# Kernel tuning notes

Hardware: AMD Instinct MI355X
Metric: run time of the kernel (lower is better)

## Reference

```python
import jax, jax.numpy as jnp
import numpy as np

DIM = 512; H = 8; DH = 64; M = 256; ITERS = 6; K = 33  # residual conv kernel


def _pinv(x, iters=ITERS):
    # Moore-Penrose iterative pseudo-inverse (lucidrains moore_penrose_iter_pinv)
    abs_x = jnp.abs(x)
    denom = abs_x.sum(-1).max() * abs_x.sum(-2).max()  # global max of col/row sums
    z = jnp.swapaxes(x, -1, -2) / denom
    I = jnp.eye(x.shape[-1], dtype=x.dtype)
    for _ in range(iters):
        xz = x @ z
        z = 0.25 * z @ (13. * I - xz @ (15. * I - xz @ (7. * I - xz)))
    return z


def setup_inputs() -> dict:
    key = jax.random.key(0)
    ks = jax.random.split(key, 5)
    b, n = 4, 4096
    inner = H * DH
    x = jax.random.normal(ks[0], (b, n, DIM), jnp.float32)
    ln_g = jnp.ones((DIM,), jnp.float32)
    ln_b = jnp.zeros((DIM,), jnp.float32)
    w_qkv = jax.random.normal(ks[1], (DIM, 3 * inner), jnp.float32) / np.sqrt(DIM).astype(np.float32)
    w_out = jax.random.normal(ks[2], (inner, DIM), jnp.float32) / np.sqrt(inner).astype(np.float32)
    b_out = jnp.zeros((DIM,), jnp.float32)
    res_w = jax.random.normal(ks[3], (H, K), jnp.float32) * 0.02  # depthwise conv weight per head
    return {"x": x, "ln_g": ln_g, "ln_b": ln_b, "w_qkv": w_qkv,
            "w_out": w_out, "b_out": b_out, "res_w": res_w}


def reference(x, ln_g, ln_b, w_qkv, w_out, b_out, res_w):
    b, n, d = x.shape
    # LayerNorm (eps=1e-5, biased variance, like torch)
    mu = x.mean(-1, keepdims=True)
    var = ((x - mu) ** 2).mean(-1, keepdims=True)
    xn = (x - mu) * jax.lax.rsqrt(var + 1e-5) * ln_g + ln_b
    # QKV projection, no bias
    qkv = xn @ w_qkv  # [b, n, 3*h*dh]
    q, k, v = jnp.split(qkv, 3, axis=-1)
    tohd = lambda t: t.reshape(b, n, H, DH).transpose(0, 2, 1, 3)  # b h n d
    q = tohd(q) * (DH ** -0.5)
    k = tohd(k)
    v = tohd(v)
    # landmarks: mean over consecutive blocks of l = n // M (n divisible by M here)
    l = n // M
    q_l = q.reshape(b, H, M, l, DH).mean(3)  # b h m d
    k_l = k.reshape(b, H, M, l, DH).mean(3)
    attn1 = jax.nn.softmax(jnp.einsum('bhid,bhjd->bhij', q, k_l), axis=-1)   # b h n m
    attn2 = jax.nn.softmax(jnp.einsum('bhid,bhjd->bhij', q_l, k_l), axis=-1)  # b h m m
    attn3 = jax.nn.softmax(jnp.einsum('bhid,bhjd->bhij', q_l, k), axis=-1)   # b h m n
    out = (attn1 @ _pinv(attn2)) @ (attn3 @ v)  # b h n dh
    # depthwise residual conv over sequence dim (Conv2d(heads, heads, (33,1), groups=heads))
    res = jax.lax.conv_general_dilated(
        v, res_w.reshape(H, 1, K, 1), (1, 1), ((K // 2, K // 2), (0, 0)),
        feature_group_count=H, dimension_numbers=('NCHW', 'OIHW', 'NCHW'))
    out = out + res
    # merge heads + output projection (dropout is identity at eval)
    out = out.transpose(0, 2, 1, 3).reshape(b, n, H * DH) @ w_out + b_out
    # TransLayer residual
    return x + out
```

## Files before the change

### kernel.cpp

```cpp
#include <hip/hip_runtime.h>
#include <hip/hip_bf16.h>

#define SEQ    4096
#define NBAT   4
#define NHEAD  8
#define NBH    32
#define DMODEL 512
#define DHEAD  64
#define NLM    256

typedef __attribute__((ext_vector_type(8))) short s8v;
typedef __attribute__((ext_vector_type(4))) float f4v;

__device__ __forceinline__ float b2f(unsigned short u){
  union { unsigned int i; float f; } v; v.i = ((unsigned int)u) << 16; return v.f;
}
__device__ __forceinline__ unsigned short f2b(float f){
  union { float f; unsigned int i; } v; v.f = f;
  unsigned int r = v.i + 0x7fffu + ((v.i >> 16) & 1u);
  return (unsigned short)(r >> 16);
}
__device__ __forceinline__ s8v ldg8(const unsigned short* p){
  return *reinterpret_cast<const s8v*>(p);
}
__device__ __forceinline__ f4v mfma16(s8v a, s8v b, f4v c){
  return __builtin_amdgcn_mfma_f32_16x16x32_bf16(a, b, c, 0, 0, 0);
}
__device__ __forceinline__ f4v zero4(){ f4v z; z[0]=0.f; z[1]=0.f; z[2]=0.f; z[3]=0.f; return z; }
__device__ __forceinline__ void gload16(const unsigned short* g, unsigned short* l){
  __builtin_amdgcn_global_load_lds((const __attribute__((address_space(1))) unsigned int*)g,
                                   (__attribute__((address_space(3))) unsigned int*)l, 16, 0, 0);
}

__global__ void k_prep(const float* __restrict__ wqkv, const float* __restrict__ wout,
                       unsigned short* __restrict__ wqkvT, unsigned short* __restrict__ woutT,
                       unsigned int* __restrict__ denomU){
  int t = blockIdx.x*256 + threadIdx.x;
  if (t == 0) denomU[0] = 0u;
  if (t < 786432){ int kk = t/1536, n = t%1536; wqkvT[(size_t)n*512 + kk] = f2b(wqkv[t]); }
  else { int t2 = t - 786432; if (t2 < 262144){ int kk = t2/512, n = t2%512; woutT[(size_t)n*512 + kk] = f2b(wout[t2]); } }
}

__global__ __launch_bounds__(256) void k_ln(const float* __restrict__ x, const float* __restrict__ g,
                                            const float* __restrict__ be, unsigned short* __restrict__ xn){
  int row = blockIdx.x*4 + (threadIdx.x>>6);
  int l = threadIdx.x & 63;
  const float* xr = x + (size_t)row*DMODEL;
  float4 a = *(const float4*)(xr + l*4);
  float4 b = *(const float4*)(xr + 256 + l*4);
  float s = a.x+a.y+a.z+a.w + b.x+b.y+b.z+b.w;
  float q = a.x*a.x+a.y*a.y+a.z*a.z+a.w*a.w + b.x*b.x+b.y*b.y+b.z*b.z+b.w*b.w;
  #pragma unroll
  for (int m=1;m<64;m<<=1){ s += __shfl_xor(s,m); q += __shfl_xor(q,m); }
  float mean = s*(1.f/DMODEL);
  float rstd = rsqrtf(q*(1.f/DMODEL) - mean*mean + 1e-5f);
  int c0 = l*4, c1 = 256 + l*4;
  float av[4] = {a.x,a.y,a.z,a.w}, bv[4] = {b.x,b.y,b.z,b.w};
  ushort4 u0, u1;
  unsigned short* p0 = (unsigned short*)&u0; unsigned short* p1 = (unsigned short*)&u1;
  #pragma unroll
  for (int e=0;e<4;++e){
    p0[e] = f2b((av[e]-mean)*rstd*g[c0+e] + be[c0+e]);
    p1[e] = f2b((bv[e]-mean)*rstd*g[c1+e] + be[c1+e]);
  }
  *(ushort4*)(xn + (size_t)row*DMODEL + c0) = u0;
  *(ushort4*)(xn + (size_t)row*DMODEL + c1) = u1;
}

__device__ __forceinline__ void gemm512v2(const unsigned short* __restrict__ A, const unsigned short* __restrict__ B,
                                          int m0, int n0, int t, unsigned short* lA, unsigned short* lB,
                                          f4v acc[4][4]){
  int w = t>>6, l = t&63;
  int wm = (w&1)*64, wn = (w>>1)*64;
  int g = l>>4, qi = l&15;
  int rs = (w<<4) + (l>>2);
  int s0 = l&3;
  int c0 = ((s0 ^ ((rs>>1)&3)) << 3);
  int r1 = rs + 64;
  int c1 = ((s0 ^ ((r1>>1)&3)) << 3);
  const unsigned short* gA0 = A + (size_t)(m0+rs)*DMODEL + c0;
  const unsigned short* gA1 = A + (size_t)(m0+r1)*DMODEL + c1;
  const unsigned short* gB0 = B + (size_t)(n0+rs)*DMODEL + c0;
  const unsigned short* gB1 = B + (size_t)(n0+r1)*DMODEL + c1;
  unsigned short* dA0 = lA + (w<<9);
  unsigned short* dA1 = lA + 2048 + (w<<9);
  unsigned short* dB0 = lB + (w<<9);
  unsigned short* dB1 = lB + 2048 + (w<<9);
  int aofs[4], bofs[4];
  #pragma unroll
  for (int i=0;i<4;++i){
    int ra = wm + i*16 + qi;
    aofs[i] = ra*32 + ((g ^ ((ra>>1)&3))<<3);
    int rb = wn + i*16 + qi;
    bofs[i] = rb*32 + ((g ^ ((rb>>1)&3))<<3);
  }
  for (int ks=0; ks<16; ++ks){
    gload16(gA0, dA0); gload16(gA1, dA1);
    gload16(gB0, dB0); gload16(gB1, dB1);
    gA0 += 32; gA1 += 32; gB0 += 32; gB1 += 32;
    __syncthreads();
    s8v af[4], bf[4];
    #pragma unroll
    for (int i=0;i<4;++i) af[i] = *(s8v*)&lA[aofs[i]];
    #pragma unroll
    for (int j=0;j<4;++j) bf[j] = *(s8v*)&lB[bofs[j]];
    #pragma unroll
    for (int i=0;i<4;++i)
      #pragma unroll
      for (int j=0;j<4;++j) acc[i][j] = mfma16(af[i], bf[j], acc[i][j]);
    __syncthreads();
  }
}

__global__ __launch_bounds__(256) void k_gqkv(const unsigned short* __restrict__ xn, const unsigned short* __restrict__ wT,
                                              unsigned short* __restrict__ q, unsigned short* __restrict__ k,
                                              unsigned short* __restrict__ v, unsigned short* __restrict__ vT){
  __shared__ __align__(16) unsigned short lA[4096], lB[4096];
  int bid = blockIdx.x; int mblk = bid/12, nblk = bid%12;
  int m0 = mblk*128, n0 = nblk*128;
  int t = threadIdx.x;
  f4v acc[4][4];
  #pragma unroll
  for (int i=0;i<4;++i)
    #pragma unroll
    for (int j=0;j<4;++j) acc[i][j] = zero4();
  gemm512v2(xn, wT, m0, n0, t, lA, lB, acc);
  int w = t>>6, l = t&63; int wm = (w&1)*64, wn = (w>>1)*64;
  int part = nblk >> 2;
  int coff = (nblk & 3) * 128;
  unsigned short* dst = (part==0) ? q : (part==1) ? k : v;
  float scale = (part==0) ? 0.125f : 1.f;
  #pragma unroll
  for (int i=0;i<4;++i)
  #pragma unroll
  for (int j=0;j<4;++j){
    int colg = coff + wn + j*16 + (l&15);
    int h = colg>>6, c = colg&63;
    #pragma unroll
    for (int r=0;r<4;++r){
      int rowg = m0 + wm + i*16 + ((l>>4)<<2) + r;
      int b = rowg>>12, n = rowg&4095;
      unsigned short val = f2b(acc[i][j][r]*scale);
      dst[ (((size_t)(b*NHEAD + h))*SEQ + n)*DHEAD + c ] = val;
      if (part == 2)
        vT[ (((size_t)(b*NHEAD + h))*DHEAD + c)*SEQ + n ] = val;
    }
  }
}

__global__ __launch_bounds__(256) void k_gout(const unsigned short* __restrict__ ao, const unsigned short* __restrict__ wT,
                                              const float* __restrict__ x, const float* __restrict__ bo,
                                              float* __restrict__ out){
  __shared__ __align__(16) unsigned short lA[4096], lB[4096];
  int bid = blockIdx.x; int mblk = bid>>2, nblk = bid&3;
  int m0 = mblk*128, n0 = nblk*128;
  int t = threadIdx.x;
  f4v acc[4][4];
  #pragma unroll
  for (int i=0;i<4;++i)
    #pragma unroll
    for (int j=0;j<4;++j) acc[i][j] = zero4();
  gemm512v2(ao, wT, m0, n0, t, lA, lB, acc);
  int w = t>>6, l = t&63; int wm = (w&1)*64, wn = (w>>1)*64;
  #pragma unroll
  for (int i=0;i<4;++i)
  #pragma unroll
  for (int j=0;j<4;++j){
    int colg = n0 + wn + j*16 + (l&15);
    #pragma unroll
    for (int r=0;r<4;++r){
      int rowg = m0 + wm + i*16 + ((l>>4)<<2) + r;
      size_t ad = (size_t)rowg*DMODEL + colg;
      out[ad] = acc[i][j][r] + x[ad] + bo[colg];
    }
  }
}

__global__ void k_lmk(const unsigned short* __restrict__ q, const unsigned short* __restrict__ k,
                      unsigned short* __restrict__ ql, unsigned short* __restrict__ kl){
  int tg = blockIdx.x*256 + threadIdx.x;
  int c4 = (tg&15)*4, m = (tg>>4)&255, bh = tg>>12;
  const unsigned short* qb = q + ((size_t)bh*SEQ + m*16)*DHEAD + c4;
  const unsigned short* kb = k + ((size_t)bh*SEQ + m*16)*DHEAD + c4;
  float s0=0.f,s1=0.f,s2=0.f,s3=0.f, t0=0.f,t1=0.f,t2=0.f,t3=0.f;
  #pragma unroll
  for (int j=0;j<16;++j){
    ushort4 uq = *(const ushort4*)(qb + (size_t)j*DHEAD);
    ushort4 uk = *(const ushort4*)(kb + (size_t)j*DHEAD);
    s0+=b2f(uq.x); s1+=b2f(uq.y); s2+=b2f(uq.z); s3+=b2f(uq.w);
    t0+=b2f(uk.x); t1+=b2f(uk.y); t2+=b2f(uk.z); t3+=b2f(uk.w);
  }
  ushort4 oq, ok;
  oq.x=f2b(s0*(1.f/16.f)); oq.y=f2b(s1*(1.f/16.f)); oq.z=f2b(s2*(1.f/16.f)); oq.w=f2b(s3*(1.f/16.f));
  ok.x=f2b(t0*(1.f/16.f)); ok.y=f2b(t1*(1.f/16.f)); ok.z=f2b(t2*(1.f/16.f)); ok.w=f2b(t3*(1.f/16.f));
  *(ushort4*)(ql + ((size_t)bh*NLM + m)*DHEAD + c4) = oq;
  *(ushort4*)(kl + ((size_t)bh*NLM + m)*DHEAD + c4) = ok;
}

__global__ __launch_bounds__(512) void k_attn2(const unsigned short* __restrict__ ql, const unsigned short* __restrict__ kl,
                                               unsigned short* __restrict__ a2, unsigned short* __restrict__ a2t,
                                               unsigned int* __restrict__ denomU){
  __shared__ float cs[256];
  int bh = blockIdx.x; int t = threadIdx.x; int w = t>>6, l = t&63;
  const unsigned short* Q = ql + (size_t)bh*NLM*DHEAD;
  const unsigned short* K = kl + (size_t)bh*NLM*DHEAD;
  f4v acc[2][16];
  #pragma unroll
  for (int i=0;i<2;++i)
    #pragma unroll
    for (int j=0;j<16;++j) acc[i][j] = zero4();
  int m0 = w*32;
  #pragma unroll
  for (int ks=0; ks<2; ++ks){
    int kk = ks*32 + ((l>>4)<<3);
    s8v af0 = ldg8(&Q[(size_t)(m0 + (l&15))*DHEAD + kk]);
    s8v af1 = ldg8(&Q[(size_t)(m0 + 16 + (l&15))*DHEAD + kk]);
    #pragma unroll
    for (int j=0;j<16;++j){
      s8v bf = ldg8(&K[(size_t)(j*16 + (l&15))*DHEAD + kk]);
      acc[0][j] = mfma16(af0, bf, acc[0][j]);
      acc[1][j] = mfma16(af1, bf, acc[1][j]);
    }
  }
  #pragma unroll
  for (int i=0;i<2;++i)
  #pragma unroll
  for (int r=0;r<4;++r){
    float mx = -1e30f;
    #pragma unroll
    for (int j=0;j<16;++j) mx = fmaxf(mx, acc[i][j][r]);
    #pragma unroll
    for (int mm=1;mm<16;mm<<=1) mx = fmaxf(mx, __shfl_xor(mx,mm));
    float sm = 0.f;
    #pragma unroll
    for (int j=0;j<16;++j){ float p = __expf(acc[i][j][r]-mx); acc[i][j][r]=p; sm += p; }
    #pragma unroll
    for (int mm=1;mm<16;mm<<=1) sm += __shfl_xor(sm,mm);
    float inv = 1.f/sm;
    #pragma unroll
    for (int j=0;j<16;++j) acc[i][j][r] *= inv;
  }
  for (int e=t; e<256; e+=512) cs[e] = 0.f;
  __syncthreads();
  size_t b0 = (size_t)bh*NLM*NLM;
  #pragma unroll
  for (int i=0;i<2;++i)
  #pragma unroll
  for (int j=0;j<16;++j){
    int col = j*16 + (l&15);
    int rowb = m0 + i*16 + ((l>>4)<<2);
    float csp = 0.f;
    #pragma unroll
    for (int r=0;r<4;++r){
      float p = acc[i][j][r];
      unsigned short pb = f2b(p);
      a2 [b0 + (size_t)(rowb+r)*NLM + col] = pb;
      a2t[b0 + (size_t)col*NLM + rowb + r] = pb;
      csp += p;
    }
    csp += __shfl_xor(csp, 16); csp += __shfl_xor(csp, 32);
    if ((l>>4) == 0) atomicAdd(&cs[col], csp);
  }
  __syncthreads();
  if (t < 256) atomicMax(denomU, __float_as_uint(cs[t]));
}

__global__ __launch_bounds__(128) void k_a3w2(const unsigned short* __restrict__ ql, const unsigned short* __restrict__ kb,
                                              const unsigned short* __restrict__ vT, unsigned short* __restrict__ w2t){
  int bh = blockIdx.x >> 3;
  int t = threadIdx.x, w = t>>6, l = t&63;
  int q0 = ((blockIdx.x & 7) << 5) + (w<<4);
  int g = l>>4, qi = l&15;
  const unsigned short* Q = ql + ((size_t)bh*NLM + q0)*DHEAD;
  const unsigned short* K = kb + (size_t)bh*SEQ*DHEAD;
  const unsigned short* V = vT + (size_t)bh*DHEAD*SEQ;
  float m_run = -1e30f, den = 0.f;
  f4v oacc[4];
  #pragma unroll
  for (int j=0;j<4;++j) oacc[j] = zero4();
  int sl0 = ((g&1)*2)*16 + qi;
  int jsel = g>>1;
  for (int kc=0; kc<16; ++kc){
    const unsigned short* Kc = K + (size_t)kc*256*DHEAD;
    f4v acc[16];
    #pragma unroll
    for (int j=0;j<16;++j) acc[j] = zero4();
    #pragma unroll
    for (int ks=0;ks<2;++ks){
      int kk = ks*32 + g*8;
      s8v bq = ldg8(&Q[(size_t)qi*DHEAD + kk]);
      #pragma unroll
      for (int j=0;j<16;++j){
        s8v ak = ldg8(&Kc[(size_t)(j*16+qi)*DHEAD + kk]);
        acc[j] = mfma16(ak, bq, acc[j]);
      }
    }
    float cm = -1e30f;
    #pragma unroll
    for (int j=0;j<16;++j)
      cm = fmaxf(cm, fmaxf(fmaxf(acc[j][0],acc[j][1]), fmaxf(acc[j][2],acc[j][3])));
    cm = fmaxf(cm, __shfl_xor(cm,16));
    cm = fmaxf(cm, __shfl_xor(cm,32));
    float nm = fmaxf(m_run, cm);
    float f = __expf(m_run - nm);
    m_run = nm;
    float ls = 0.f;
    unsigned int pku[32];
    #pragma unroll
    for (int j=0;j<16;++j){
      float p0 = __expf(acc[j][0]-nm), p1 = __expf(acc[j][1]-nm);
      float p2 = __expf(acc[j][2]-nm), p3 = __expf(acc[j][3]-nm);
      ls += (p0+p1)+(p2+p3);
      pku[2*j+0] = (unsigned int)f2b(p0) | ((unsigned int)f2b(p1)<<16);
      pku[2*j+1] = (unsigned int)f2b(p2) | ((unsigned int)f2b(p3)<<16);
    }
    den = den*f + ls;
    float fr0 = __shfl(f, g*4+0, 64), fr1 = __shfl(f, g*4+1, 64);
    float fr2 = __shfl(f, g*4+2, 64), fr3 = __shfl(f, g*4+3, 64);
    #pragma unroll
    for (int j=0;j<4;++j){
      oacc[j][0]*=fr0; oacc[j][1]*=fr1; oacc[j][2]*=fr2; oacc[j][3]*=fr3;
    }
    #pragma unroll
    for (int ks=0;ks<8;++ks){
      unsigned int w0a = (unsigned int)__shfl((int)pku[4*ks+0], sl0, 64);
      unsigned int w1a = (unsigned int)__shfl((int)pku[4*ks+1], sl0, 64);
      unsigned int w0b = (unsigned int)__shfl((int)pku[4*ks+2], sl0, 64);
      unsigned int w1b = (unsigned int)__shfl((int)pku[4*ks+3], sl0, 64);
      unsigned int w2a = (unsigned int)__shfl((int)pku[4*ks+0], sl0+16, 64);
      unsigned int w3a = (unsigned int)__shfl((int)pku[4*ks+1], sl0+16, 64);
      unsigned int w2b = (unsigned int)__shfl((int)pku[4*ks+2], sl0+16, 64);
      unsigned int w3b = (unsigned int)__shfl((int)pku[4*ks+3], sl0+16, 64);
      unsigned int wv0 = jsel ? w0b : w0a;
      unsigned int wv1 = jsel ? w1b : w1a;
      unsigned int wv2 = jsel ? w2b : w2a;
      unsigned int wv3 = jsel ? w3b : w3a;
      s8v af;
      af[0] = (short)(wv0&0xffff); af[1] = (short)(wv0>>16);
      af[2] = (short)(wv1&0xffff); af[3] = (short)(wv1>>16);
      af[4] = (short)(wv2&0xffff); af[5] = (short)(wv2>>16);
      af[6] = (short)(wv3&0xffff); af[7] = (short)(wv3>>16);
      int mk = ks*32 + g*8;
      #pragma unroll
      for (int j=0;j<4;++j){
        s8v bu = ldg8(&V[(size_t)(j*16+qi)*SEQ + kc*256 + mk]);
        oacc[j] = mfma16(af, bu, oacc[j]);
      }
    }
  }
  den += __shfl_xor(den,16); den += __shfl_xor(den,32);
  float inv = 1.f/den;
  float ir0 = __shfl(inv, g*4+0, 64), ir1 = __shfl(inv, g*4+1, 64);
  float ir2 = __shfl(inv, g*4+2, 64), ir3 = __shfl(inv, g*4+3, 64);
  #pragma unroll
  for (int j=0;j<4;++j){
    size_t cb = ((size_t)bh*DHEAD + j*16 + qi)*NLM + q0 + g*4;
    w2t[cb+0] = f2b(oacc[j][0]*ir0);
    w2t[cb+1] = f2b(oacc[j][1]*ir1);
    w2t[cb+2] = f2b(oacc[j][2]*ir2);
    w2t[cb+3] = f2b(oacc[j][3]*ir3);
  }
}

__global__ __launch_bounds__(256) void k_conv(const unsigned short* __restrict__ v, const float* __restrict__ rw,
                                              unsigned short* __restrict__ cf){
  int bh = blockIdx.x >> 6;
  int n0 = (blockIdx.x & 63) * 64;
  int h = bh & 7, b = bh >> 3;
  int t = threadIdx.x;
  int tx = t & 15, ty = t >> 4;
  int c4 = tx * 4;
  int nb = n0 + ty * 4;
  const unsigned short* vb = v + ((size_t)bh * SEQ) * DHEAD + c4;
  ushort4 val[36];
  #pragma unroll
  for (int i = 0; i < 36; ++i){
    int nn = nb - 16 + i;
    if (nn >= 0 && nn < SEQ) val[i] = *(const ushort4*)(vb + (size_t)nn * DHEAD);
    else { val[i].x = 0; val[i].y = 0; val[i].z = 0; val[i].w = 0; }
  }
  float wgt[33];
  #pragma unroll
  for (int o = 0; o < 33; ++o) wgt[o] = rw[h*33 + o];
  #pragma unroll
  for (int i = 0; i < 4; ++i){
    float s0 = 0.f, s1 = 0.f, s2 = 0.f, s3 = 0.f;
    #pragma unroll
    for (int o = 0; o < 33; ++o){
      ushort4 u = val[i + o];
      float w0 = wgt[o];
      s0 += w0 * b2f(u.x); s1 += w0 * b2f(u.y);
      s2 += w0 * b2f(u.z); s3 += w0 * b2f(u.w);
    }
    ushort4 ov;
    ov.x = f2b(s0); ov.y = f2b(s1); ov.z = f2b(s2); ov.w = f2b(s3);
    size_t ad = ((size_t)b * SEQ + (nb + i)) * DMODEL + h * DHEAD + c4;
    *(ushort4*)(cf + ad) = ov;
  }
}

__device__ __forceinline__ void pcore(const unsigned short* __restrict__ Ab, const unsigned short* __restrict__ Bb,
                                      int m0, int n0, int l, f4v acc[4][4]){
  for (int ks=0; ks<8; ++ks){
    int kk = ks*32 + ((l>>4)<<3);
    s8v af[4], bf[4];
    #pragma unroll
    for (int i=0;i<4;++i) af[i] = ldg8(&Ab[(size_t)(m0 + i*16 + (l&15))*256 + kk]);
    #pragma unroll
    for (int j=0;j<4;++j) bf[j] = ldg8(&Bb[(size_t)(n0 + j*16 + (l&15))*256 + kk]);
    #pragma unroll
    for (int i=0;i<4;++i)
      #pragma unroll
      for (int j=0;j<4;++j) acc[i][j] = mfma16(af[i], bf[j], acc[i][j]);
  }
}

__global__ __launch_bounds__(64) void k_pg1(const unsigned short* __restrict__ A, const unsigned short* __restrict__ BT,
                                            unsigned short* __restrict__ oN, unsigned short* __restrict__ oT,
                                            int sdiv, const unsigned int* __restrict__ denomU){
  int bid = blockIdx.x;
  int bh = bid>>4, tt = bid&15;
  int m0 = (tt>>2)*64, n0 = (tt&3)*64;
  int l = threadIdx.x;
  const unsigned short* Ab = A + (size_t)bh*65536;
  const unsigned short* Bb = BT + (size_t)bh*65536;
  f4v acc[4][4];
  #pragma unroll
  for (int i=0;i<4;++i)
    #pragma unroll
    for (int j=0;j<4;++j) acc[i][j] = zero4();
  pcore(Ab, Bb, m0, n0, l, acc);
  float s = sdiv ? 1.f/__uint_as_float(denomU[0]) : 1.f;
  #pragma unroll
  for (int i=0;i<4;++i)
  #pragma unroll
  for (int j=0;j<4;++j){
    int col = n0 + j*16 + (l&15);
    #pragma unroll
    for (int r=0;r<4;++r){
      int row = m0 + i*16 + ((l>>4)<<2) + r;
      unsigned short ob = f2b(acc[i][j][r]*s);
      oN[(size_t)bh*65536 + (size_t)row*256 + col] = ob;
      oT[(size_t)bh*65536 + (size_t)col*256 + row] = ob;
    }
  }
}

__global__ __launch_bounds__(64) void k_pg2(const unsigned short* __restrict__ xzN, const unsigned short* __restrict__ xzT,
                                            const unsigned short* __restrict__ zsrc,
                                            unsigned short* __restrict__ CT, unsigned short* __restrict__ PN,
                                            int sdiv, const unsigned int* __restrict__ denomU){
  int bid = blockIdx.x;
  int part = bid>>9; bid &= 511;
  int bh = bid>>4, tt = bid&15;
  int m0 = (tt>>2)*64, n0 = (tt&3)*64;
  int l = threadIdx.x;
  const unsigned short* Ab = (part==0 ? xzN : zsrc) + (size_t)bh*65536;
  const unsigned short* Bb = xzT + (size_t)bh*65536;
  f4v acc[4][4];
  #pragma unroll
  for (int i=0;i<4;++i)
    #pragma unroll
    for (int j=0;j<4;++j) acc[i][j] = zero4();
  pcore(Ab, Bb, m0, n0, l, acc);
  if (part == 0){
    #pragma unroll
    for (int i=0;i<4;++i)
    #pragma unroll
    for (int j=0;j<4;++j){
      int col = n0 + j*16 + (l&15);
      #pragma unroll
      for (int r=0;r<4;++r){
        int row = m0 + i*16 + ((l>>4)<<2) + r;
        float xv = b2f(xzN[(size_t)bh*65536 + (size_t)row*256 + col]);
        CT[(size_t)bh*65536 + (size_t)col*256 + row] = f2b(7.f*xv - acc[i][j][r]);
      }
    }
  } else {
    float s = sdiv ? 1.f/__uint_as_float(denomU[0]) : 1.f;
    #pragma unroll
    for (int i=0;i<4;++i)
    #pragma unroll
    for (int j=0;j<4;++j){
      int col = n0 + j*16 + (l&15);
      #pragma unroll
      for (int r=0;r<4;++r){
        int row = m0 + i*16 + ((l>>4)<<2) + r;
        PN[(size_t)bh*65536 + (size_t)row*256 + col] = f2b(acc[i][j][r]*s);
      }
    }
  }
}

__global__ __launch_bounds__(64) void k_pg3(const unsigned short* __restrict__ PN, const unsigned short* __restrict__ CT,
                                            const unsigned short* __restrict__ zsrc,
                                            unsigned short* __restrict__ zN, unsigned short* __restrict__ zT,
                                            int sdiv, const unsigned int* __restrict__ denomU){
  int bid = blockIdx.x;
  int bh = bid>>4, tt = bid&15;
  int m0 = (tt>>2)*64, n0 = (tt&3)*64;
  int l = threadIdx.x;
  const unsigned short* Ab = PN + (size_t)bh*65536;
  const unsigned short* Bb = CT + (size_t)bh*65536;
  f4v acc[4][4];
  #pragma unroll
  for (int i=0;i<4;++i)
    #pragma unroll
    for (int j=0;j<4;++j) acc[i][j] = zero4();
  pcore(Ab, Bb, m0, n0, l, acc);
  float zs = sdiv ? 1.f/__uint_as_float(denomU[0]) : 1.f;
  #pragma unroll
  for (int i=0;i<4;++i)
  #pragma unroll
  for (int j=0;j<4;++j){
    int col = n0 + j*16 + (l&15);
    #pragma unroll
    for (int r=0;r<4;++r){
      int row = m0 + i*16 + ((l>>4)<<2) + r;
      float zv = b2f(zsrc[(size_t)bh*65536 + (size_t)row*256 + col])*zs;
      float pv = b2f(PN  [(size_t)bh*65536 + (size_t)row*256 + col]);
      float res = 0.25f*(13.f*zv - 15.f*pv + acc[i][j][r]);
      unsigned short ob = f2b(res);
      zN[(size_t)bh*65536 + (size_t)row*256 + col] = ob;
      zT[(size_t)bh*65536 + (size_t)col*256 + row] = ob;
    }
  }
}

template<bool WN, bool WT>
__global__ __launch_bounds__(64) void k_pgemm(
    const unsigned short* __restrict__ A, const unsigned short* __restrict__ BT,
    unsigned short* __restrict__ oN, unsigned short* __restrict__ oT,
    int mt, int nt, long strA, long strBT, long strON, long strOT)
{
  int bid = blockIdx.x;
  int nper = mt*nt;
  int bh = bid/nper, tt = bid%nper;
  int m0 = (tt/nt)*64, n0 = (tt%nt)*64;
  const unsigned short* Ab = A + (size_t)bh*strA;
  const unsigned short* Bb = BT + (size_t)bh*strBT;
  int l = threadIdx.x;
  f4v acc[4][4];
  #pragma unroll
  for (int i=0;i<4;++i)
    #pragma unroll
    for (int j=0;j<4;++j) acc[i][j] = zero4();
  pcore(Ab, Bb, m0, n0, l, acc);
  #pragma unroll
  for (int i=0;i<4;++i)
  #pragma unroll
  for (int j=0;j<4;++j){
    int col = n0 + j*16 + (l&15);
    #pragma unroll
    for (int r=0;r<4;++r){
      int row = m0 + i*16 + ((l>>4)<<2) + r;
      unsigned short ob = f2b(acc[i][j][r]);
      if constexpr (WN) oN[(size_t)bh*strON + (size_t)row*256 + col] = ob;
      if constexpr (WT) oT[(size_t)bh*strOT + (size_t)col*256 + row] = ob;
    }
  }
}

__global__ __launch_bounds__(256) void k_attn1(const unsigned short* __restrict__ qb, const unsigned short* __restrict__ kl,
                                               const unsigned short* __restrict__ ut, const unsigned short* __restrict__ cf,
                                               unsigned short* __restrict__ ao){
  int bh = blockIdx.x>>6;
  int t = threadIdx.x, w = t>>6, l = t&63;
  int q0 = ((blockIdx.x&63)<<6) + (w<<4);
  int g = l>>4, qi = l&15;
  const unsigned short* Q = qb + (size_t)bh*SEQ*DHEAD;
  const unsigned short* K = kl + (size_t)bh*NLM*DHEAD;
  f4v acc[16];
  #pragma unroll
  for (int j=0;j<16;++j) acc[j] = zero4();
  #pragma unroll
  for (int ks=0;ks<2;++ks){
    int kk = ks*32 + g*8;
    s8v bq = ldg8(&Q[(size_t)(q0+qi)*DHEAD + kk]);
    #pragma unroll
    for (int j=0;j<16;++j){
      s8v ak = ldg8(&K[(size_t)(j*16+qi)*DHEAD + kk]);
      acc[j] = mfma16(ak, bq, acc[j]);
    }
  }
  float mx = -1e30f;
  #pragma unroll
  for (int j=0;j<16;++j)
    mx = fmaxf(mx, fmaxf(fmaxf(acc[j][0],acc[j][1]), fmaxf(acc[j][2],acc[j][3])));
  mx = fmaxf(mx, __shfl_xor(mx,16));
  mx = fmaxf(mx, __shfl_xor(mx,32));
  float sm = 0.f;
  #pragma unroll
  for (int j=0;j<16;++j)
    #pragma unroll
    for (int r=0;r<4;++r){ float p = __expf(acc[j][r]-mx); acc[j][r]=p; sm += p; }
  sm += __shfl_xor(sm,16); sm += __shfl_xor(sm,32);
  float inv = 1.f/sm;
  unsigned int pku[32];
  #pragma unroll
  for (int j=0;j<16;++j){
    pku[2*j+0] = (unsigned int)f2b(acc[j][0]*inv) | ((unsigned int)f2b(acc[j][1]*inv)<<16);
    pku[2*j+1] = (unsigned int)f2b(acc[j][2]*inv) | ((unsigned int)f2b(acc[j][3]*inv)<<16);
  }
  const unsigned short* U = ut + (size_t)bh*DHEAD*NLM;
  f4v oacc[4];
  #pragma unroll
  for (int j=0;j<4;++j) oacc[j] = zero4();
  int sl0 = ((g&1)*2)*16 + qi;
  int jsel = g>>1;
  #pragma unroll
  for (int ks=0;ks<8;++ks){
    unsigned int w0a = (unsigned int)__shfl((int)pku[4*ks+0], sl0, 64);
    unsigned int w1a = (unsigned int)__shfl((int)pku[4*ks+1], sl0, 64);
    unsigned int w0b = (unsigned int)__shfl((int)pku[4*ks+2], sl0, 64);
    unsigned int w1b = (unsigned int)__shfl((int)pku[4*ks+3], sl0, 64);
    unsigned int w2a = (unsigned int)__shfl((int)pku[4*ks+0], sl0+16, 64);
    unsigned int w3a = (unsigned int)__shfl((int)pku[4*ks+1], sl0+16, 64);
    unsigned int w2b = (unsigned int)__shfl((int)pku[4*ks+2], sl0+16, 64);
    unsigned int w3b = (unsigned int)__shfl((int)pku[4*ks+3], sl0+16, 64);
    unsigned int wv0 = jsel ? w0b : w0a;
    unsigned int wv1 = jsel ? w1b : w1a;
    unsigned int wv2 = jsel ? w2b : w2a;
    unsigned int wv3 = jsel ? w3b : w3a;
    s8v af;
    af[0] = (short)(wv0&0xffff); af[1] = (short)(wv0>>16);
    af[2] = (short)(wv1&0xffff); af[3] = (short)(wv1>>16);
    af[4] = (short)(wv2&0xffff); af[5] = (short)(wv2>>16);
    af[6] = (short)(wv3&0xffff); af[7] = (short)(wv3>>16);
    int mk = ks*32 + g*8;
    #pragma unroll
    for (int j=0;j<4;++j){
      s8v bu = ldg8(&U[(size_t)(j*16+qi)*NLM + mk]);
      oacc[j] = mfma16(af, bu, oacc[j]);
    }
  }
  int b = bh>>3, h = bh&7;
  #pragma unroll
  for (int j=0;j<4;++j){
    int c = j*16 + qi;
    #pragma unroll
    for (int r=0;r<4;++r){
      int n = q0 + g*4 + r;
      size_t ad = ((size_t)(b*SEQ + n))*DMODEL + h*DHEAD + c;
      ao[ad] = f2b(oacc[j][r] + b2f(cf[ad]));
    }
  }
}

extern "C" void kernel_launch(void* const* d_in, const int* in_sizes, int n_in,
                              void* d_out, int out_size, void* d_ws, size_t ws_size,
                              hipStream_t stream){
  const float* x    = (const float*)d_in[0];
  const float* lng  = (const float*)d_in[1];
  const float* lnb  = (const float*)d_in[2];
  const float* wqkv = (const float*)d_in[3];
  const float* wout = (const float*)d_in[4];
  const float* bout = (const float*)d_in[5];
  const float* resw = (const float*)d_in[6];
  float* out = (float*)d_out;

  char* ws = (char*)d_ws;
  size_t off = 0;
  auto alloc = [&](size_t bytes)->char*{ char* p = ws + off; off += (bytes + 255) & ~(size_t)255; return p; };

  unsigned short* wqkvT = (unsigned short*)alloc((size_t)1536*512*2);
  unsigned short* woutT = (unsigned short*)alloc((size_t)512*512*2);
  unsigned int*   denomU= (unsigned int*)  alloc(256);
  unsigned short* xn    = (unsigned short*)alloc((size_t)16384*512*2);
  unsigned short* zA  = xn;
  unsigned short* zAT = xn + (size_t)1*NBH*NLM*NLM;
  unsigned short* zB  = xn + (size_t)2*NBH*NLM*NLM;
  unsigned short* zBT = xn + (size_t)3*NBH*NLM*NLM;
  unsigned short* q   = (unsigned short*)alloc((size_t)NBH*SEQ*DHEAD*2);
  unsigned short* kb  = (unsigned short*)alloc((size_t)NBH*SEQ*DHEAD*2);
  unsigned short* ao  = kb;
  unsigned short* v   = (unsigned short*)alloc((size_t)NBH*SEQ*DHEAD*2);
  unsigned short* vT  = (unsigned short*)alloc((size_t)NBH*DHEAD*SEQ*2);
  unsigned short* ql  = (unsigned short*)alloc((size_t)NBH*NLM*DHEAD*2);
  unsigned short* kl  = (unsigned short*)alloc((size_t)NBH*NLM*DHEAD*2);
  unsigned short* a2  = (unsigned short*)alloc((size_t)NBH*NLM*NLM*2);
  unsigned short* a2t = (unsigned short*)alloc((size_t)NBH*NLM*NLM*2);
  unsigned short* convf = (unsigned short*)alloc((size_t)NBAT*SEQ*DMODEL*2);
  unsigned short* xz  = (unsigned short*)alloc((size_t)NBH*NLM*NLM*2);
  unsigned short* xzt = (unsigned short*)alloc((size_t)NBH*NLM*NLM*2);
  unsigned short* pn  = (unsigned short*)alloc((size_t)NBH*NLM*NLM*2);
  unsigned short* ctb = (unsigned short*)alloc((size_t)NBH*NLM*NLM*2);
  unsigned short* w2t = (unsigned short*)alloc((size_t)NBH*DHEAD*NLM*2);
  unsigned short* ut  = (unsigned short*)alloc((size_t)NBH*DHEAD*NLM*2);
  (void)ws_size; (void)in_sizes; (void)n_in; (void)out_size;

  k_prep<<<4096,256,0,stream>>>(wqkv, wout, wqkvT, woutT, denomU);
  k_ln  <<<4096,256,0,stream>>>(x, lng, lnb, xn);
  k_gqkv<<<1536,256,0,stream>>>(xn, wqkvT, q, kb, v, vT);
  k_lmk <<<512,256,0,stream>>>(q, kb, ql, kl);
  k_attn2<<<32,512,0,stream>>>(ql, kl, a2, a2t, denomU);
  k_a3w2<<<256,128,0,stream>>>(ql, kb, vT, w2t);
  k_conv<<<2048,256,0,stream>>>(v, resw, convf);

  unsigned short* zN_[2] = {zA, zB};
  unsigned short* zT_[2] = {zAT, zBT};
  for (int it = 0; it < 6; ++it){
    const unsigned short* BT   = (it==0) ? a2  : zT_[(it-1)&1];
    const unsigned short* zsrc = (it==0) ? a2t : zN_[(it-1)&1];
    int sdiv = (it==0) ? 1 : 0;
    k_pg1<<<512 ,64,0,stream>>>(a2, BT, xz, xzt, sdiv, denomU);
    k_pg2<<<1024,64,0,stream>>>(xz, xzt, zsrc, ctb, pn, sdiv, denomU);
    k_pg3<<<512 ,64,0,stream>>>(pn, ctb, zsrc, zN_[it&1], zT_[it&1], sdiv, denomU);
  }
  k_pgemm<false,true><<<128,64,0,stream>>>(zN_[1], w2t, (unsigned short*)nullptr, ut, 4,1, 65536L,16384L,0L,16384L);

  k_attn1<<<2048,256,0,stream>>>(q, kl, ut, convf, ao);
  k_gout <<<512,256,0,stream>>>(ao, woutT, x, bout, out);
}
```

Baseline: 559.6 us.

## Split-K the attn3·V landmark kernel and widen pinv GEMM blocks to four waves

The attn3@V kernel becomes split-K with a flash-decoding style design: 1024 blocks each handle a quarter of the sequence and write float partial outputs, running maxima and denominators. A new combine kernel rescales the partials, merges them and writes w2t in bf16. The pseudo-inverse GEMM kernels and the final z·W2 GEMM now run four 16-row waves per 64x64 tile instead of one wave computing the whole tile, which adds parallelism to latency-bound small GEMMs. The cost is an extra launch, partial-buffer round trips, and each wave loading the B operand separately without LDS sharing.

```diff
diff --git a/kernel.cpp b/kernel.cpp
--- a/kernel.cpp
+++ b/kernel.cpp
@@ -265,11 +265,14 @@
   if (t < 256) atomicMax(denomU, __float_as_uint(cs[t]));
 }
 
-__global__ __launch_bounds__(128) void k_a3w2(const unsigned short* __restrict__ ql, const unsigned short* __restrict__ kb,
-                                              const unsigned short* __restrict__ vT, unsigned short* __restrict__ w2t){
-  int bh = blockIdx.x >> 3;
+__global__ __launch_bounds__(128) void k_a3w2p(const unsigned short* __restrict__ ql, const unsigned short* __restrict__ kb,
+                                               const unsigned short* __restrict__ vT,
+                                               float* __restrict__ po, float* __restrict__ pm, float* __restrict__ pd){
+  int ksp = blockIdx.x & 3;
+  int qb  = (blockIdx.x >> 2) & 7;
+  int bh  = blockIdx.x >> 5;
   int t = threadIdx.x, w = t>>6, l = t&63;
-  int q0 = ((blockIdx.x & 7) << 5) + (w<<4);
+  int q0 = (qb<<5) + (w<<4);
   int g = l>>4, qi = l&15;
   const unsigned short* Q = ql + ((size_t)bh*NLM + q0)*DHEAD;
   const unsigned short* K = kb + (size_t)bh*SEQ*DHEAD;
@@ -280,7 +283,7 @@
   for (int j=0;j<4;++j) oacc[j] = zero4();
   int sl0 = ((g&1)*2)*16 + qi;
   int jsel = g>>1;
-  for (int kc=0; kc<16; ++kc){
+  for (int kc = ksp*4; kc < ksp*4+4; ++kc){
     const unsigned short* Kc = K + (size_t)kc*256*DHEAD;
     f4v acc[16];
     #pragma unroll
@@ -349,17 +352,40 @@
     }
   }
   den += __shfl_xor(den,16); den += __shfl_xor(den,32);
-  float inv = 1.f/den;
-  float ir0 = __shfl(inv, g*4+0, 64), ir1 = __shfl(inv, g*4+1, 64);
-  float ir2 = __shfl(inv, g*4+2, 64), ir3 = __shfl(inv, g*4+3, 64);
-  #pragma unroll
-  for (int j=0;j<4;++j){
-    size_t cb = ((size_t)bh*DHEAD + j*16 + qi)*NLM + q0 + g*4;
-    w2t[cb+0] = f2b(oacc[j][0]*ir0);
-    w2t[cb+1] = f2b(oacc[j][1]*ir1);
-    w2t[cb+2] = f2b(oacc[j][2]*ir2);
-    w2t[cb+3] = f2b(oacc[j][3]*ir3);
-  }
+  #pragma unroll
+  for (int j=0;j<4;++j)
+    #pragma unroll
+    for (int r=0;r<4;++r)
+      po[(((size_t)(ksp*NBH + bh))*NLM + q0 + g*4 + r)*DHEAD + j*16 + qi] = oacc[j][r];
+  if (g == 0){
+    pm[(size_t)(ksp*NBH + bh)*NLM + q0 + qi] = m_run;
+    pd[(size_t)(ksp*NBH + bh)*NLM + q0 + qi] = den;
+  }
+}
+
+__global__ __launch_bounds__(256) void k_a3c(const float* __restrict__ po, const float* __restrict__ pm,
+                                             const float* __restrict__ pd, unsigned short* __restrict__ w2t){
+  int tg = blockIdx.x*256 + threadIdx.x;
+  int bh = tg >> 12; int c = (tg >> 6) & 63; int r4 = (tg & 63) << 2;
+  ushort4 ov;
+  unsigned short* op = (unsigned short*)&ov;
+  #pragma unroll
+  for (int rr=0; rr<4; ++rr){
+    int row = r4 + rr;
+    float m[4];
+    float gm = -1e30f;
+    #pragma unroll
+    for (int s=0;s<4;++s){ m[s] = pm[(size_t)(s*NBH+bh)*NLM + row]; gm = fmaxf(gm, m[s]); }
+    float den = 0.f, o = 0.f;
+    #pragma unroll
+    for (int s=0;s<4;++s){
+      float wsc = __expf(m[s]-gm);
+      den += pd[(size_t)(s*NBH+bh)*NLM + row]*wsc;
+      o   += po[(((size_t)(s*NBH+bh))*NLM + row)*DHEAD + c]*wsc;
+    }
+    op[rr] = f2b(o/den);
+  }
+  *(ushort4*)&w2t[(size_t)bh*DHEAD*NLM + (size_t)c*NLM + r4] = ov;
 }
 
 __global__ __launch_bounds__(256) void k_conv(const unsigned short* __restrict__ v, const float* __restrict__ rw,
@@ -399,166 +425,127 @@
   }
 }
 
-__device__ __forceinline__ void pcore(const unsigned short* __restrict__ Ab, const unsigned short* __restrict__ Bb,
-                                      int m0, int n0, int l, f4v acc[4][4]){
-  for (int ks=0; ks<8; ++ks){
-    int kk = ks*32 + ((l>>4)<<3);
-    s8v af[4], bf[4];
-    #pragma unroll
-    for (int i=0;i<4;++i) af[i] = ldg8(&Ab[(size_t)(m0 + i*16 + (l&15))*256 + kk]);
-    #pragma unroll
-    for (int j=0;j<4;++j) bf[j] = ldg8(&Bb[(size_t)(n0 + j*16 + (l&15))*256 + kk]);
-    #pragma unroll
-    for (int i=0;i<4;++i)
-      #pragma unroll
-      for (int j=0;j<4;++j) acc[i][j] = mfma16(af[i], bf[j], acc[i][j]);
-  }
-}
-
-__global__ __launch_bounds__(64) void k_pg1(const unsigned short* __restrict__ A, const unsigned short* __restrict__ BT,
-                                            unsigned short* __restrict__ oN, unsigned short* __restrict__ oT,
+__device__ __forceinline__ void grow16(const unsigned short* __restrict__ A, const unsigned short* __restrict__ BT,
+                                       int rowb, int n0, int qi, int g, f4v acc[4]){
+  #pragma unroll
+  for (int ks=0;ks<8;++ks){
+    int kk = ks*32 + g*8;
+    s8v af = ldg8(&A[(size_t)(rowb+qi)*256 + kk]);
+    #pragma unroll
+    for (int j=0;j<4;++j){
+      s8v bf = ldg8(&BT[(size_t)(n0+j*16+qi)*256 + kk]);
+      acc[j] = mfma16(af, bf, acc[j]);
+    }
+  }
+}
+
+
+__global__ __launch_bounds__(256) void k_q1(const unsigned short* __restrict__ a2, const unsigned short* __restrict__ zT,
+                                            unsigned short* __restrict__ xzN, unsigned short* __restrict__ xzT,
                                             int sdiv, const unsigned int* __restrict__ denomU){
-  int bid = blockIdx.x;
-  int bh = bid>>4, tt = bid&15;
+  int blk = blockIdx.x;
+  int t = threadIdx.x, w = t>>6, l = t&63, g = l>>4, qi = l&15;
+  int bh = blk>>4, tt = blk&15;
   int m0 = (tt>>2)*64, n0 = (tt&3)*64;
-  int l = threadIdx.x;
-  const unsigned short* Ab = A + (size_t)bh*65536;
-  const unsigned short* Bb = BT + (size_t)bh*65536;
-  f4v acc[4][4];
-  #pragma unroll
-  for (int i=0;i<4;++i)
-    #pragma unroll
-    for (int j=0;j<4;++j) acc[i][j] = zero4();
-  pcore(Ab, Bb, m0, n0, l, acc);
+  size_t bb = (size_t)bh*65536;
+  int rowb = m0 + w*16;
   float s = sdiv ? 1.f/__uint_as_float(denomU[0]) : 1.f;
-  #pragma unroll
-  for (int i=0;i<4;++i)
-  #pragma unroll
-  for (int j=0;j<4;++j){
-    int col = n0 + j*16 + (l&15);
+  f4v acc[4];
+  #pragma unroll
+  for (int j=0;j<4;++j) acc[j] = zero4();
+  grow16(a2+bb, zT+bb, rowb, n0, qi, g, acc);
+  #pragma unroll
+  for (int j=0;j<4;++j)
     #pragma unroll
     for (int r=0;r<4;++r){
-      int row = m0 + i*16 + ((l>>4)<<2) + r;
-      unsigned short ob = f2b(acc[i][j][r]*s);
-      oN[(size_t)bh*65536 + (size_t)row*256 + col] = ob;
-      oT[(size_t)bh*65536 + (size_t)col*256 + row] = ob;
-    }
-  }
-}
-
-__global__ __launch_bounds__(64) void k_pg2(const unsigned short* __restrict__ xzN, const unsigned short* __restrict__ xzT,
+      int row = rowb+g*4+r, col = n0+j*16+qi;
+      unsigned short ob = f2b(acc[j][r]*s);
+      xzN[bb + (size_t)row*256 + col] = ob;
+      xzT[bb + (size_t)col*256 + row] = ob;
+    }
+}
+
+__global__ __launch_bounds__(256) void k_q2(const unsigned short* __restrict__ xzN, const unsigned short* __restrict__ xzT,
                                             const unsigned short* __restrict__ zsrc,
                                             unsigned short* __restrict__ CT, unsigned short* __restrict__ PN,
                                             int sdiv, const unsigned int* __restrict__ denomU){
-  int bid = blockIdx.x;
-  int part = bid>>9; bid &= 511;
-  int bh = bid>>4, tt = bid&15;
+  int blk = blockIdx.x;
+  int part = blk>>9; blk &= 511;
+  int t = threadIdx.x, w = t>>6, l = t&63, g = l>>4, qi = l&15;
+  int bh = blk>>4, tt = blk&15;
   int m0 = (tt>>2)*64, n0 = (tt&3)*64;
-  int l = threadIdx.x;
-  const unsigned short* Ab = (part==0 ? xzN : zsrc) + (size_t)bh*65536;
-  const unsigned short* Bb = xzT + (size_t)bh*65536;
-  f4v acc[4][4];
-  #pragma unroll
-  for (int i=0;i<4;++i)
-    #pragma unroll
-    for (int j=0;j<4;++j) acc[i][j] = zero4();
-  pcore(Ab, Bb, m0, n0, l, acc);
+  size_t bb = (size_t)bh*65536;
+  int rowb = m0 + w*16;
+  f4v acc[4];
+  #pragma unroll
+  for (int j=0;j<4;++j) acc[j] = zero4();
   if (part == 0){
-    #pragma unroll
-    for (int i=0;i<4;++i)
-    #pragma unroll
-    for (int j=0;j<4;++j){
-      int col = n0 + j*16 + (l&15);
+    grow16(xzN+bb, xzT+bb, rowb, n0, qi, g, acc);
+    #pragma unroll
+    for (int j=0;j<4;++j)
       #pragma unroll
       for (int r=0;r<4;++r){
-        int row = m0 + i*16 + ((l>>4)<<2) + r;
-        float xv = b2f(xzN[(size_t)bh*65536 + (size_t)row*256 + col]);
-        CT[(size_t)bh*65536 + (size_t)col*256 + row] = f2b(7.f*xv - acc[i][j][r]);
+        int row = rowb+g*4+r, col = n0+j*16+qi;
+        float xv = b2f(xzN[bb + (size_t)row*256 + col]);
+        CT[bb + (size_t)col*256 + row] = f2b(7.f*xv - acc[j][r]);
       }
-    }
   } else {
+    grow16(zsrc+bb, xzT+bb, rowb, n0, qi, g, acc);
     float s = sdiv ? 1.f/__uint_as_float(denomU[0]) : 1.f;
     #pragma unroll
-    for (int i=0;i<4;++i)
-    #pragma unroll
-    for (int j=0;j<4;++j){
-      int col = n0 + j*16 + (l&15);
+    for (int j=0;j<4;++j)
       #pragma unroll
       for (int r=0;r<4;++r){
-        int row = m0 + i*16 + ((l>>4)<<2) + r;
-        PN[(size_t)bh*65536 + (size_t)row*256 + col] = f2b(acc[i][j][r]*s);
+        int row = rowb+g*4+r, col = n0+j*16+qi;
+        PN[bb + (size_t)row*256 + col] = f2b(acc[j][r]*s);
       }
-    }
-  }
-}
-
-__global__ __launch_bounds__(64) void k_pg3(const unsigned short* __restrict__ PN, const unsigned short* __restrict__ CT,
+  }
+}
+
+__global__ __launch_bounds__(256) void k_q3(const unsigned short* __restrict__ PN, const unsigned short* __restrict__ CT,
                                             const unsigned short* __restrict__ zsrc,
                                             unsigned short* __restrict__ zN, unsigned short* __restrict__ zT,
                                             int sdiv, const unsigned int* __restrict__ denomU){
-  int bid = blockIdx.x;
-  int bh = bid>>4, tt = bid&15;
+  int blk = blockIdx.x;
+  int t = threadIdx.x, w = t>>6, l = t&63, g = l>>4, qi = l&15;
+  int bh = blk>>4, tt = blk&15;
   int m0 = (tt>>2)*64, n0 = (tt&3)*64;
-  int l = threadIdx.x;
-  const unsigned short* Ab = PN + (size_t)bh*65536;
-  const unsigned short* Bb = CT + (size_t)bh*65536;
-  f4v acc[4][4];
-  #pragma unroll
-  for (int i=0;i<4;++i)
-    #pragma unroll
-    for (int j=0;j<4;++j) acc[i][j] = zero4();
-  pcore(Ab, Bb, m0, n0, l, acc);
+  size_t bb = (size_t)bh*65536;
+  int rowb = m0 + w*16;
   float zs = sdiv ? 1.f/__uint_as_float(denomU[0]) : 1.f;
-  #pragma unroll
-  for (int i=0;i<4;++i)
-  #pragma unroll
-  for (int j=0;j<4;++j){
-    int col = n0 + j*16 + (l&15);
+  f4v acc[4];
+  #pragma unroll
+  for (int j=0;j<4;++j) acc[j] = zero4();
+  grow16(PN+bb, CT+bb, rowb, n0, qi, g, acc);
+  #pragma unroll
+  for (int j=0;j<4;++j)
     #pragma unroll
     for (int r=0;r<4;++r){
-      int row = m0 + i*16 + ((l>>4)<<2) + r;
-      float zv = b2f(zsrc[(size_t)bh*65536 + (size_t)row*256 + col])*zs;
-      float pv = b2f(PN  [(size_t)bh*65536 + (size_t)row*256 + col]);
-      float res = 0.25f*(13.f*zv - 15.f*pv + acc[i][j][r]);
+      int row = rowb+g*4+r, col = n0+j*16+qi;
+      size_t idx = bb + (size_t)row*256 + col;
+      float zv = b2f(zsrc[idx])*zs;
+      float pv = b2f(PN[idx]);
+      float res = 0.25f*(13.f*zv - 15.f*pv + acc[j][r]);
       unsigned short ob = f2b(res);
-      zN[(size_t)bh*65536 + (size_t)row*256 + col] = ob;
-      zT[(size_t)bh*65536 + (size_t)col*256 + row] = ob;
-    }
-  }
-}
-
-template<bool WN, bool WT>
-__global__ __launch_bounds__(64) void k_pgemm(
-    const unsigned short* __restrict__ A, const unsigned short* __restrict__ BT,
-    unsigned short* __restrict__ oN, unsigned short* __restrict__ oT,
-    int mt, int nt, long strA, long strBT, long strON, long strOT)
-{
-  int bid = blockIdx.x;
-  int nper = mt*nt;
-  int bh = bid/nper, tt = bid%nper;
-  int m0 = (tt/nt)*64, n0 = (tt%nt)*64;
-  const unsigned short* Ab = A + (size_t)bh*strA;
-  const unsigned short* Bb = BT + (size_t)bh*strBT;
-  int l = threadIdx.x;
-  f4v acc[4][4];
-  #pragma unroll
-  for (int i=0;i<4;++i)
-    #pragma unroll
-    for (int j=0;j<4;++j) acc[i][j] = zero4();
-  pcore(Ab, Bb, m0, n0, l, acc);
-  #pragma unroll
-  for (int i=0;i<4;++i)
-  #pragma unroll
-  for (int j=0;j<4;++j){
-    int col = n0 + j*16 + (l&15);
-    #pragma unroll
-    for (int r=0;r<4;++r){
-      int row = m0 + i*16 + ((l>>4)<<2) + r;
-      unsigned short ob = f2b(acc[i][j][r]);
-      if constexpr (WN) oN[(size_t)bh*strON + (size_t)row*256 + col] = ob;
-      if constexpr (WT) oT[(size_t)bh*strOT + (size_t)col*256 + row] = ob;
-    }
-  }
+      zN[idx] = ob;
+      zT[bb + (size_t)col*256 + row] = ob;
+    }
+}
+
+__global__ __launch_bounds__(256) void k_ue(const unsigned short* __restrict__ w2t, const unsigned short* __restrict__ z6N,
+                                            unsigned short* __restrict__ ut){
+  int blk = blockIdx.x;
+  int t = threadIdx.x, w = t>>6, l = t&63, g = l>>4, qi = l&15;
+  int bh = blk>>2, n0 = (blk&3)*64;
+  f4v acc[4];
+  #pragma unroll
+  for (int j=0;j<4;++j) acc[j] = zero4();
+  grow16(w2t + (size_t)bh*16384, z6N + (size_t)bh*65536, w*16, n0, qi, g, acc);
+  #pragma unroll
+  for (int j=0;j<4;++j)
+    #pragma unroll
+    for (int r=0;r<4;++r)
+      ut[(size_t)bh*16384 + (size_t)(w*16+g*4+r)*256 + n0+j*16+qi] = f2b(acc[j][r]);
 }
 
 __global__ __launch_bounds__(256) void k_attn1(const unsigned short* __restrict__ qb, const unsigned short* __restrict__ kl,
@@ -681,10 +668,13 @@
   unsigned short* a2  = (unsigned short*)alloc((size_t)NBH*NLM*NLM*2);
   unsigned short* a2t = (unsigned short*)alloc((size_t)NBH*NLM*NLM*2);
   unsigned short* convf = (unsigned short*)alloc((size_t)NBAT*SEQ*DMODEL*2);
-  unsigned short* xz  = (unsigned short*)alloc((size_t)NBH*NLM*NLM*2);
-  unsigned short* xzt = (unsigned short*)alloc((size_t)NBH*NLM*NLM*2);
+  unsigned short* xzN = (unsigned short*)alloc((size_t)NBH*NLM*NLM*2);
+  unsigned short* xzT = (unsigned short*)alloc((size_t)NBH*NLM*NLM*2);
   unsigned short* pn  = (unsigned short*)alloc((size_t)NBH*NLM*NLM*2);
   unsigned short* ctb = (unsigned short*)alloc((size_t)NBH*NLM*NLM*2);
+  float* po = (float*)alloc((size_t)4*NBH*NLM*DHEAD*4);
+  float* pm = (float*)alloc((size_t)4*NBH*NLM*4);
+  float* pd = (float*)alloc((size_t)4*NBH*NLM*4);
   unsigned short* w2t = (unsigned short*)alloc((size_t)NBH*DHEAD*NLM*2);
   unsigned short* ut  = (unsigned short*)alloc((size_t)NBH*DHEAD*NLM*2);
   (void)ws_size; (void)in_sizes; (void)n_in; (void)out_size;
@@ -694,7 +684,8 @@
   k_gqkv<<<1536,256,0,stream>>>(xn, wqkvT, q, kb, v, vT);
   k_lmk <<<512,256,0,stream>>>(q, kb, ql, kl);
   k_attn2<<<32,512,0,stream>>>(ql, kl, a2, a2t, denomU);
-  k_a3w2<<<256,128,0,stream>>>(ql, kb, vT, w2t);
+  k_a3w2p<<<1024,128,0,stream>>>(ql, kb, vT, po, pm, pd);
+  k_a3c <<<512,256,0,stream>>>(po, pm, pd, w2t);
   k_conv<<<2048,256,0,stream>>>(v, resw, convf);
 
   unsigned short* zN_[2] = {zA, zB};
@@ -703,11 +694,11 @@
     const unsigned short* BT   = (it==0) ? a2  : zT_[(it-1)&1];
     const unsigned short* zsrc = (it==0) ? a2t : zN_[(it-1)&1];
     int sdiv = (it==0) ? 1 : 0;
-    k_pg1<<<512 ,64,0,stream>>>(a2, BT, xz, xzt, sdiv, denomU);
-    k_pg2<<<1024,64,0,stream>>>(xz, xzt, zsrc, ctb, pn, sdiv, denomU);
-    k_pg3<<<512 ,64,0,stream>>>(pn, ctb, zsrc, zN_[it&1], zT_[it&1], sdiv, denomU);
-  }
-  k_pgemm<false,true><<<128,64,0,stream>>>(zN_[1], w2t, (unsigned short*)nullptr, ut, 4,1, 65536L,16384L,0L,16384L);
+    k_q1<<<512 ,256,0,stream>>>(a2, BT, xzN, xzT, sdiv, denomU);
+    k_q2<<<1024,256,0,stream>>>(xzN, xzT, zsrc, ctb, pn, sdiv, denomU);
+    k_q3<<<512 ,256,0,stream>>>(pn, ctb, zsrc, zN_[it&1], zT_[it&1], sdiv, denomU);
+  }
+  k_ue<<<128,256,0,stream>>>(w2t, zN_[1], ut);
 
   k_attn1<<<2048,256,0,stream>>>(q, kl, ut, convf, ao);
   k_gout <<<512,256,0,stream>>>(ao, woutT, x, bout, out);
```

Result: slower. 578.0 us (+3.3%).

## Split attn3·V over key chunks with a merge kernel; swizzle GEMM block order

Applied to the files above, without the earlier changes.

The landmark-query attention over the full sequence (k_a3w2) previously ran as only 256 blocks, each looping over all 16 key chunks. It is now split four ways along the key dimension (1024 blocks). Each split writes fp32 partial outputs plus its running max and denominator, and a new k_a3c kernel merges them flash-decoding style. The QKV and output-projection GEMMs also remap block indices so consecutive blocks are spread across M tiles. The aim is to fill more compute units on the low-parallelism stage, at the cost of an extra launch and fp32 partial traffic.

```diff
diff --git a/kernel.cpp b/kernel.cpp
--- a/kernel.cpp
+++ b/kernel.cpp
@@ -8,6 +8,7 @@
 #define DMODEL 512
 #define DHEAD  64
 #define NLM    256
+#define NSP    4
 
 typedef __attribute__((ext_vector_type(8))) short s8v;
 typedef __attribute__((ext_vector_type(4))) float f4v;
@@ -116,7 +117,9 @@
                                               unsigned short* __restrict__ q, unsigned short* __restrict__ k,
                                               unsigned short* __restrict__ v, unsigned short* __restrict__ vT){
   __shared__ __align__(16) unsigned short lA[4096], lB[4096];
-  int bid = blockIdx.x; int mblk = bid/12, nblk = bid%12;
+  int b0 = blockIdx.x;
+  int bid = (b0 & 7) * 192 + (b0 >> 3);
+  int mblk = bid/12, nblk = bid%12;
   int m0 = mblk*128, n0 = nblk*128;
   int t = threadIdx.x;
   f4v acc[4][4];
@@ -152,7 +155,9 @@
                                               const float* __restrict__ x, const float* __restrict__ bo,
                                               float* __restrict__ out){
   __shared__ __align__(16) unsigned short lA[4096], lB[4096];
-  int bid = blockIdx.x; int mblk = bid>>2, nblk = bid&3;
+  int b0 = blockIdx.x;
+  int bid = (b0 & 7) * 64 + (b0 >> 3);
+  int mblk = bid>>2, nblk = bid&3;
   int m0 = mblk*128, n0 = nblk*128;
   int t = threadIdx.x;
   f4v acc[4][4];
@@ -265,11 +270,14 @@
   if (t < 256) atomicMax(denomU, __float_as_uint(cs[t]));
 }
 
-__global__ __launch_bounds__(128) void k_a3w2(const unsigned short* __restrict__ ql, const unsigned short* __restrict__ kb,
-                                              const unsigned short* __restrict__ vT, unsigned short* __restrict__ w2t){
-  int bh = blockIdx.x >> 3;
+__global__ __launch_bounds__(128) void k_a3w2p(const unsigned short* __restrict__ ql, const unsigned short* __restrict__ kb,
+                                               const unsigned short* __restrict__ vT,
+                                               float* __restrict__ po, float* __restrict__ pm, float* __restrict__ pd){
+  int ksp = blockIdx.x & 3;
+  int qb  = (blockIdx.x >> 2) & 7;
+  int bh  = blockIdx.x >> 5;
   int t = threadIdx.x, w = t>>6, l = t&63;
-  int q0 = ((blockIdx.x & 7) << 5) + (w<<4);
+  int q0 = (qb<<5) + (w<<4);
   int g = l>>4, qi = l&15;
   const unsigned short* Q = ql + ((size_t)bh*NLM + q0)*DHEAD;
   const unsigned short* K = kb + (size_t)bh*SEQ*DHEAD;
@@ -280,7 +288,7 @@
   for (int j=0;j<4;++j) oacc[j] = zero4();
   int sl0 = ((g&1)*2)*16 + qi;
   int jsel = g>>1;
-  for (int kc=0; kc<16; ++kc){
+  for (int kc = ksp*4; kc < ksp*4+4; ++kc){
     const unsigned short* Kc = K + (size_t)kc*256*DHEAD;
     f4v acc[16];
     #pragma unroll
@@ -349,17 +357,40 @@
     }
   }
   den += __shfl_xor(den,16); den += __shfl_xor(den,32);
-  float inv = 1.f/den;
-  float ir0 = __shfl(inv, g*4+0, 64), ir1 = __shfl(inv, g*4+1, 64);
-  float ir2 = __shfl(inv, g*4+2, 64), ir3 = __shfl(inv, g*4+3, 64);
-  #pragma unroll
-  for (int j=0;j<4;++j){
-    size_t cb = ((size_t)bh*DHEAD + j*16 + qi)*NLM + q0 + g*4;
-    w2t[cb+0] = f2b(oacc[j][0]*ir0);
-    w2t[cb+1] = f2b(oacc[j][1]*ir1);
-    w2t[cb+2] = f2b(oacc[j][2]*ir2);
-    w2t[cb+3] = f2b(oacc[j][3]*ir3);
-  }
+  #pragma unroll
+  for (int j=0;j<4;++j)
+    #pragma unroll
+    for (int r=0;r<4;++r)
+      po[(((size_t)(ksp*NBH + bh))*NLM + q0 + g*4 + r)*DHEAD + j*16 + qi] = oacc[j][r];
+  if (g == 0){
+    pm[(size_t)(ksp*NBH + bh)*NLM + q0 + qi] = m_run;
+    pd[(size_t)(ksp*NBH + bh)*NLM + q0 + qi] = den;
+  }
+}
+
+__global__ __launch_bounds__(256) void k_a3c(const float* __restrict__ po, const float* __restrict__ pm,
+                                             const float* __restrict__ pd, unsigned short* __restrict__ w2t){
+  int tg = blockIdx.x*256 + threadIdx.x;
+  int bh = tg >> 12; int c = (tg >> 6) & 63; int r4 = (tg & 63) << 2;
+  ushort4 ov;
+  unsigned short* op = (unsigned short*)&ov;
+  #pragma unroll
+  for (int rr=0; rr<4; ++rr){
+    int row = r4 + rr;
+    float m[NSP];
+    float gm = -1e30f;
+    #pragma unroll
+    for (int s=0;s<NSP;++s){ m[s] = pm[(size_t)(s*NBH+bh)*NLM + row]; gm = fmaxf(gm, m[s]); }
+    float den = 0.f, o = 0.f;
+    #pragma unroll
+    for (int s=0;s<NSP;++s){
+      float wsc = __expf(m[s]-gm);
+      den += pd[(size_t)(s*NBH+bh)*NLM + row]*wsc;
+      o   += po[(((size_t)(s*NBH+bh))*NLM + row)*DHEAD + c]*wsc;
+    }
+    op[rr] = f2b(o/den);
+  }
+  *(ushort4*)&w2t[(size_t)bh*DHEAD*NLM + (size_t)c*NLM + r4] = ov;
 }
 
 __global__ __launch_bounds__(256) void k_conv(const unsigned short* __restrict__ v, const float* __restrict__ rw,
@@ -681,10 +712,13 @@
   unsigned short* a2  = (unsigned short*)alloc((size_t)NBH*NLM*NLM*2);
   unsigned short* a2t = (unsigned short*)alloc((size_t)NBH*NLM*NLM*2);
   unsigned short* convf = (unsigned short*)alloc((size_t)NBAT*SEQ*DMODEL*2);
-  unsigned short* xz  = (unsigned short*)alloc((size_t)NBH*NLM*NLM*2);
-  unsigned short* xzt = (unsigned short*)alloc((size_t)NBH*NLM*NLM*2);
+  unsigned short* xzN = (unsigned short*)alloc((size_t)NBH*NLM*NLM*2);
+  unsigned short* xzT = (unsigned short*)alloc((size_t)NBH*NLM*NLM*2);
   unsigned short* pn  = (unsigned short*)alloc((size_t)NBH*NLM*NLM*2);
   unsigned short* ctb = (unsigned short*)alloc((size_t)NBH*NLM*NLM*2);
+  float* po = (float*)alloc((size_t)NSP*NBH*NLM*DHEAD*4);
+  float* pm = (float*)alloc((size_t)NSP*NBH*NLM*4);
+  float* pd = (float*)alloc((size_t)NSP*NBH*NLM*4);
   unsigned short* w2t = (unsigned short*)alloc((size_t)NBH*DHEAD*NLM*2);
   unsigned short* ut  = (unsigned short*)alloc((size_t)NBH*DHEAD*NLM*2);
   (void)ws_size; (void)in_sizes; (void)n_in; (void)out_size;
@@ -694,7 +728,8 @@
   k_gqkv<<<1536,256,0,stream>>>(xn, wqkvT, q, kb, v, vT);
   k_lmk <<<512,256,0,stream>>>(q, kb, ql, kl);
   k_attn2<<<32,512,0,stream>>>(ql, kl, a2, a2t, denomU);
-  k_a3w2<<<256,128,0,stream>>>(ql, kb, vT, w2t);
+  k_a3w2p<<<1024,128,0,stream>>>(ql, kb, vT, po, pm, pd);
+  k_a3c <<<512,256,0,stream>>>(po, pm, pd, w2t);
   k_conv<<<2048,256,0,stream>>>(v, resw, convf);
 
   unsigned short* zN_[2] = {zA, zB};
@@ -703,8 +738,8 @@
     const unsigned short* BT   = (it==0) ? a2  : zT_[(it-1)&1];
     const unsigned short* zsrc = (it==0) ? a2t : zN_[(it-1)&1];
     int sdiv = (it==0) ? 1 : 0;
-    k_pg1<<<512 ,64,0,stream>>>(a2, BT, xz, xzt, sdiv, denomU);
-    k_pg2<<<1024,64,0,stream>>>(xz, xzt, zsrc, ctb, pn, sdiv, denomU);
+    k_pg1<<<512 ,64,0,stream>>>(a2, BT, xzN, xzT, sdiv, denomU);
+    k_pg2<<<1024,64,0,stream>>>(xzN, xzT, zsrc, ctb, pn, sdiv, denomU);
     k_pg3<<<512 ,64,0,stream>>>(pn, ctb, zsrc, zN_[it&1], zT_[it&1], sdiv, denomU);
   }
   k_pgemm<false,true><<<128,64,0,stream>>>(zN_[1], w2t, (unsigned short*)nullptr, ut, 4,1, 65536L,16384L,0L,16384L);
```

New measurement: 497.1 us. 11.2% less time.
